# Kernel optimization log

Hardware: AMD Instinct MI355X
Metric: run time of the kernel (lower is better)

## Reference

```python
import jax, jax.numpy as jnp
import numpy as np

N = 100000   # nodes
R = 8        # relations
E = 150000   # edges per relation
D_IN = 128
D_OUT = 128
B = 2        # num_bases


def setup_inputs() -> dict:
    key = jax.random.key(0)
    ks = jax.random.split(key, 7)
    return {
        "x": jax.random.normal(ks[0], (N, D_IN), dtype=jnp.float32),
        "src": jax.random.randint(ks[1], (R, E), 0, N, dtype=jnp.int32),
        "dst": jax.random.randint(ks[2], (R, E), 0, N, dtype=jnp.int32),
        "basis_coeff": jax.random.normal(ks[3], (R, B), dtype=jnp.float32),
        "bases": jax.random.normal(ks[4], (B, D_IN, D_OUT), dtype=jnp.float32) * 0.05,
        "loop_weight": jax.random.normal(ks[5], (D_IN, D_OUT), dtype=jnp.float32) * 0.05,
        "h_bias": jax.random.normal(ks[6], (D_OUT,), dtype=jnp.float32) * 0.01,
    }


def reference(x, src, dst, basis_coeff, bases, loop_weight, h_bias):
    n = x.shape[0]
    # basis-decomposed per-relation weights: [R, D_IN, D_OUT]
    weight = jnp.einsum('rb,bio->rio', basis_coeff, bases)
    # gather src features per relation: [R, E, D_IN]
    msgs = x[src]
    # scatter-add onto dst nodes per relation (SpMM aggregate): [R, N, D_IN]
    agg = jax.vmap(lambda m, d: jax.ops.segment_sum(m, d, num_segments=n))(msgs, dst)
    # right normalization: divide by in-degree (clamped to 1), as in DGL GraphConv norm='right'
    ones = jnp.ones(src.shape[1], dtype=x.dtype)
    deg = jax.vmap(lambda d: jax.ops.segment_sum(ones, d, num_segments=n))(dst)
    agg = agg / jnp.clip(deg, 1.0)[..., None]
    # per-relation weight then sum across relations (HeteroGraphConv 'sum' agg)
    h = jnp.einsum('rni,rio->no', agg, weight)
    # self-loop + bias + activation (dropout = 0.0, eval)
    h = h + x @ loop_weight + h_bias
    return jax.nn.relu(h)
```

## Files before the change

kernel.cpp:

```cpp
#include <hip/hip_runtime.h>
#include <hip/hip_fp16.h>


#define DFEAT 128
#define NREL 8
#define ALDA 264

typedef __attribute__((ext_vector_type(8))) short bf16x8;
typedef __attribute__((ext_vector_type(4))) float f32x4;
typedef __attribute__((ext_vector_type(2))) float f32x2;

__device__ __forceinline__ ushort f2bf(float f) {
    unsigned u = __float_as_uint(f);
    u += 0x7FFF + ((u >> 16) & 1);
    return (ushort)(u >> 16);
}
__device__ __forceinline__ float bflo(unsigned u) { return __uint_as_float(u << 16); }
__device__ __forceinline__ float bfhi(unsigned u) { return __uint_as_float(u & 0xFFFF0000u); }
__device__ __forceinline__ unsigned pack2bf(float lo, float hi) {
    return (unsigned)f2bf(lo) | ((unsigned)f2bf(hi) << 16);
}

__global__ void fused_pre(const int* __restrict__ dst, int* __restrict__ deg,
                          ushort* __restrict__ rank,
                          const float* __restrict__ x, ushort* __restrict__ xb,
                          const float* __restrict__ bases, const float* __restrict__ loopw,
                          ushort* __restrict__ w2T,
                          int RE, int E, int N, int n4) {
    const int stride = gridDim.x * blockDim.x;
    const int t0 = blockIdx.x * blockDim.x + threadIdx.x;
    for (int i = t0; i < RE; i += stride) {
        int r = i / E;
        int d = dst[i];
        rank[i] = (ushort)atomicAdd(&deg[r * N + d], 1);
    }
    for (int i = t0; i < n4; i += stride) {
        float4 v = ((const float4*)x)[i];
        ushort4 o;
        o.x = f2bf(v.x); o.y = f2bf(v.y); o.z = f2bf(v.z); o.w = f2bf(v.w);
        ((ushort4*)xb)[i] = o;
    }
    for (int i = t0; i < 128 * 384; i += stride) {
        int j = i / 384, k = i % 384;
        float v = (k < 256) ? bases[(k >> 7) * DFEAT * DFEAT + (k & 127) * DFEAT + j]
                            : loopw[(k - 256) * DFEAT + j];
        w2T[i] = f2bf(v);
    }
}

__global__ void scan_block_sums(const int* __restrict__ deg, int* __restrict__ cnt,
                                int* __restrict__ bsums, int N) {
    __shared__ int sdata[256];
    int b = blockIdx.x, t = threadIdx.x;
    int idx = b * 256 + t;
    int sum = 0;
    if (idx < N) {
        #pragma unroll
        for (int r = 0; r < NREL; ++r) sum += deg[r * N + idx];
        cnt[idx] = sum;
    }
    sdata[t] = sum; __syncthreads();
    for (int s = 128; s > 0; s >>= 1) {
        if (t < s) sdata[t] += sdata[t + s];
        __syncthreads();
    }
    if (t == 0) bsums[b] = sdata[0];
}

__global__ void scan_mid(int* __restrict__ bsums, int nb) {
    __shared__ int s[256];
    int t = threadIdx.x;
    int base = t * 4;
    int v[4]; int sum = 0;
    #pragma unroll
    for (int i = 0; i < 4; ++i) {
        v[i] = sum;
        int c = (base + i < nb) ? bsums[base + i] : 0;
        sum += c;
    }
    s[t] = sum; __syncthreads();
    for (int off = 1; off < 256; off <<= 1) {
        int add = (t >= off) ? s[t - off] : 0;
        __syncthreads();
        s[t] += add;
        __syncthreads();
    }
    int excl = (t == 0) ? 0 : s[t - 1];
    #pragma unroll
    for (int i = 0; i < 4; ++i)
        if (base + i < nb) bsums[base + i] = excl + v[i];
}

__global__ void scan_write(const int* __restrict__ cnt, const int* __restrict__ bsums,
                           const int* __restrict__ deg,
                           int* __restrict__ rowStart, unsigned* __restrict__ packed,
                           int N) {
    __shared__ int tsum[256];
    int b = blockIdx.x, t = threadIdx.x;
    int idx = b * 256 + t;
    int c = (idx < N) ? cnt[idx] : 0;
    tsum[t] = c; __syncthreads();
    for (int off = 1; off < 256; off <<= 1) {
        int x = 0;
        if (t >= off) x = tsum[t - off];
        __syncthreads();
        if (t >= off) tsum[t] += x;
        __syncthreads();
    }
    int excl = (t == 0) ? 0 : tsum[t - 1];
    if (idx < N) {
        int rs = bsums[b] + excl;
        rowStart[idx] = rs;
        int pre = 0;
        #pragma unroll
        for (int r = 0; r < NREL; ++r) {
            int dv = deg[r * N + idx];
            packed[r * N + idx] = ((unsigned)(rs + pre) << 11) | (unsigned)dv;
            pre += dv;
        }
    }
}

__global__ void fill_kernel(const int* __restrict__ src, const int* __restrict__ dst,
                            const float* __restrict__ coeff,
                            const ushort* __restrict__ rank,
                            const unsigned* __restrict__ packed,
                            uint2* __restrict__ recs, int RE, int E, int N) {
    int idx = blockIdx.x * blockDim.x + threadIdx.x;
    if (idx >= RE) return;
    int r = idx / E;
    int d = dst[idx];
    unsigned p = packed[r * N + d];
    int pos = (int)(p >> 11) + (int)rank[idx];
    float inv = 1.0f / (float)(p & 2047u);
    __half2 hc = __floats2half2_rn(coeff[2 * r] * inv, coeff[2 * r + 1] * inv);
    uint2 rec;
    rec.x = (unsigned)src[idx];
    rec.y = *(unsigned*)&hc;
    recs[pos] = rec;
}

__global__ __launch_bounds__(256, 6) void gather_gemm(
    const uint2* __restrict__ recs, const int* __restrict__ rowStart,
    const int* __restrict__ cnt, const ushort* __restrict__ xb,
    const ushort* __restrict__ w2T, const float* __restrict__ bias,
    float* __restrict__ out, int N) {
    __shared__ __align__(16) ushort agg[32 * ALDA];
    const int tid = threadIdx.x;
    const int wave = tid >> 6, lane = tid & 63;
    const int q = lane >> 4;
    const int h = lane & 15;
    const int row0 = blockIdx.x * 32;

    for (int i = wave; i < 32; i += 4) {
        int d = row0 + i;
        if (d >= N) break;
        f32x2 A0 = {0.f, 0.f}, A1 = {0.f, 0.f}, A2 = {0.f, 0.f}, A3 = {0.f, 0.f};
        f32x2 B0 = {0.f, 0.f}, B1 = {0.f, 0.f}, B2 = {0.f, 0.f}, B3 = {0.f, 0.f};
        const int start = rowStart[d];
        const int len = cnt[d];
        for (int i2 = 0; i2 < len; i2 += 16) {
            uint2 r[4];
            #pragma unroll
            for (int j = 0; j < 4; ++j) {
                int e = i2 + 4 * j + q;
                r[j] = recs[start + (e < len ? e : len - 1)];
            }
            uint4 u[4];
            #pragma unroll
            for (int j = 0; j < 4; ++j)
                u[j] = *(const uint4*)(xb + (size_t)r[j].x * DFEAT + h * 8);
            #pragma unroll
            for (int j = 0; j < 4; ++j) {
                int e = i2 + 4 * j + q;
                __half2 hc = *(__half2*)&r[j].y;
                bool valid = e < len;
                float c0 = valid ? __low2float(hc) : 0.f;
                float c1 = valid ? __high2float(hc) : 0.f;
                f32x2 cc0 = {c0, c0}, cc1 = {c1, c1};
                uint4 uu = u[j];
                f32x2 f01 = {bflo(uu.x), bfhi(uu.x)};
                f32x2 f23 = {bflo(uu.y), bfhi(uu.y)};
                f32x2 f45 = {bflo(uu.z), bfhi(uu.z)};
                f32x2 f67 = {bflo(uu.w), bfhi(uu.w)};
                A0 += cc0 * f01; A1 += cc0 * f23; A2 += cc0 * f45; A3 += cc0 * f67;
                B0 += cc1 * f01; B1 += cc1 * f23; B2 += cc1 * f45; B3 += cc1 * f67;
            }
        }
        #define RED2(V) \
            V.x += __shfl_xor(V.x, 16); V.y += __shfl_xor(V.y, 16); \
            V.x += __shfl_xor(V.x, 32); V.y += __shfl_xor(V.y, 32);
        RED2(A0) RED2(A1) RED2(A2) RED2(A3)
        RED2(B0) RED2(B1) RED2(B2) RED2(B3)
        #undef RED2
        f32x2 W0 = q ? B0 : A0, W1 = q ? B1 : A1, W2 = q ? B2 : A2, W3 = q ? B3 : A3;
        uint4 w;
        w.x = pack2bf(W0.x, W0.y);
        w.y = pack2bf(W1.x, W1.y);
        w.z = pack2bf(W2.x, W2.y);
        w.w = pack2bf(W3.x, W3.y);
        if (q < 2)
            *(uint4*)(agg + i * ALDA + q * 128 + h * 8) = w;
    }
    __syncthreads();

    const int quad = lane >> 4, l16 = lane & 15;
    int arow[2];
    #pragma unroll
    for (int m = 0; m < 2; ++m) {
        int r = row0 + m * 16 + l16;
        arow[m] = (r < N) ? r : 0;
    }

    f32x4 zero = {0.f, 0.f, 0.f, 0.f};
    f32x4 acc[2][2] = {{zero, zero}, {zero, zero}};

    #pragma unroll
    for (int kt = 0; kt < 3; ++kt) {
        bf16x8 bq[4][2];
        #pragma unroll
        for (int t = 0; t < 4; ++t)
            #pragma unroll
            for (int g = 0; g < 2; ++g)
                bq[t][g] = *(const bf16x8*)(w2T + (size_t)(wave * 32 + g * 16 + l16) * 384
                                            + kt * 128 + t * 32 + quad * 8);
        #pragma unroll
        for (int m = 0; m < 2; ++m) {
            #pragma unroll
            for (int t = 0; t < 4; ++t) {
                bf16x8 a;
                if (kt < 2)
                    a = *(const bf16x8*)(agg + (m * 16 + l16) * ALDA + kt * 128 + t * 32 + quad * 8);
                else
                    a = *(const bf16x8*)(xb + (size_t)arow[m] * DFEAT + t * 32 + quad * 8);
                acc[m][0] = __builtin_amdgcn_mfma_f32_16x16x32_bf16(a, bq[t][0], acc[m][0], 0, 0, 0);
                acc[m][1] = __builtin_amdgcn_mfma_f32_16x16x32_bf16(a, bq[t][1], acc[m][1], 0, 0, 0);
            }
        }
    }

    #pragma unroll
    for (int g = 0; g < 2; ++g) {
        int c = wave * 32 + g * 16 + l16;
        float bv = bias[c];
        #pragma unroll
        for (int m = 0; m < 2; ++m) {
            #pragma unroll
            for (int reg = 0; reg < 4; ++reg) {
                int grow = row0 + m * 16 + quad * 4 + reg;
                if (grow < N)
                    out[(size_t)grow * DFEAT + c] = fmaxf(acc[m][g][reg] + bv, 0.f);
            }
        }
    }
}

extern "C" void kernel_launch(void* const* d_in, const int* in_sizes, int n_in,
                              void* d_out, int out_size, void* d_ws, size_t ws_size,
                              hipStream_t stream) {
    const float* x     = (const float*)d_in[0];
    const int*   src   = (const int*)  d_in[1];
    const int*   dst   = (const int*)  d_in[2];
    const float* coeff = (const float*)d_in[3];
    const float* bases = (const float*)d_in[4];
    const float* loopw = (const float*)d_in[5];
    const float* bias  = (const float*)d_in[6];
    float* out = (float*)d_out;

    const int N  = in_sizes[0] / DFEAT;
    const int RE = in_sizes[1];
    const int B  = in_sizes[4] / (DFEAT * DFEAT);
    const int R  = in_sizes[3] / B;
    const int E  = RE / R;
    const int NB = (N + 255) / 256;

    char* ws = (char*)d_ws;
    size_t off = 0;
    auto alloc = [&](size_t bytes) { void* p = ws + off; off = (off + bytes + 255) & ~(size_t)255; return p; };
    int*      deg      = (int*)     alloc((size_t)R * N * sizeof(int));
    ushort*   rank     = (ushort*)  alloc((size_t)RE * sizeof(ushort));
    unsigned* packed   = (unsigned*)alloc((size_t)R * N * sizeof(unsigned));
    int*      cnt      = (int*)     alloc((size_t)N * sizeof(int));
    int*      rowStart = (int*)     alloc((size_t)N * sizeof(int));
    int*      bsums    = (int*)     alloc((size_t)NB * sizeof(int));
    ushort*   w2T      = (ushort*)  alloc((size_t)128 * 384 * sizeof(ushort));
    ushort*   xb       = (ushort*)  alloc((size_t)N * DFEAT * sizeof(ushort));
    uint2*    recs     = (uint2*)   alloc((size_t)RE * sizeof(uint2));

    hipMemsetAsync(deg, 0, (size_t)R * N * sizeof(int), stream);
    fused_pre<<<4096, 256, 0, stream>>>(dst, deg, rank, x, xb, bases, loopw, w2T,
                                        RE, E, N, N * 32);
    scan_block_sums<<<NB, 256, 0, stream>>>(deg, cnt, bsums, N);
    scan_mid<<<1, 256, 0, stream>>>(bsums, NB);
    scan_write<<<NB, 256, 0, stream>>>(cnt, bsums, deg, rowStart, packed, N);
    fill_kernel<<<(RE + 255) / 256, 256, 0, stream>>>(src, dst, coeff, rank, packed,
                                                      recs, RE, E, N);

    gather_gemm<<<(N + 31) / 32, 256, 0, stream>>>(recs, rowStart, cnt, xb, w2T,
                                                   bias, out, N);
}
```

Before: 285.7 us.

## Balance edge gather across block with merge-path split and LDS float atomics

Rewrites the aggregation phase of gather_gemm so the block's contiguous edge range is split evenly among 16 thread groups, instead of assigning one destination row per wave. Each group walks its edges, tracking the local destination row encoded in the high bits of the record's src field, and flushes partial sums into an fp32 LDS tile with atomic adds. The aim is to remove load imbalance from variable in-degree and the padded, masked edge slots. In exchange it adds LDS zeroing, many LDS atomics, a serial dependent loop per thread with one edge per iteration, a larger fp32 shared tile with lower occupancy (launch bounds 6 to 4), and bf16 conversion at MFMA operand load.

Measured after the change: 408.6 us. +43.0%, slower.

```diff
diff --git a/kernel.cpp b/kernel.cpp
--- a/kernel.cpp
+++ b/kernel.cpp
@@ -4,7 +4,7 @@
 
 #define DFEAT 128
 #define NREL 8
-#define ALDA 264
+#define AF_LDA 260
 
 typedef __attribute__((ext_vector_type(8))) short bf16x8;
 typedef __attribute__((ext_vector_type(4))) float f32x4;
@@ -17,9 +17,6 @@
 }
 __device__ __forceinline__ float bflo(unsigned u) { return __uint_as_float(u << 16); }
 __device__ __forceinline__ float bfhi(unsigned u) { return __uint_as_float(u & 0xFFFF0000u); }
-__device__ __forceinline__ unsigned pack2bf(float lo, float hi) {
-    return (unsigned)f2bf(lo) | ((unsigned)f2bf(hi) << 16);
-}
 
 __global__ void fused_pre(const int* __restrict__ dst, int* __restrict__ deg,
                           ushort* __restrict__ rank,
@@ -135,72 +132,85 @@
     float inv = 1.0f / (float)(p & 2047u);
     __half2 hc = __floats2half2_rn(coeff[2 * r] * inv, coeff[2 * r + 1] * inv);
     uint2 rec;
-    rec.x = (unsigned)src[idx];
+    rec.x = (unsigned)src[idx] | ((unsigned)(d & 31) << 27);
     rec.y = *(unsigned*)&hc;
     recs[pos] = rec;
 }
 
-__global__ __launch_bounds__(256, 6) void gather_gemm(
+__global__ __launch_bounds__(256, 4) void gather_gemm(
     const uint2* __restrict__ recs, const int* __restrict__ rowStart,
-    const int* __restrict__ cnt, const ushort* __restrict__ xb,
+    const ushort* __restrict__ xb,
     const ushort* __restrict__ w2T, const float* __restrict__ bias,
-    float* __restrict__ out, int N) {
-    __shared__ __align__(16) ushort agg[32 * ALDA];
+    float* __restrict__ out, int N, int RE) {
+    __shared__ __align__(16) float aggf[32 * AF_LDA];
     const int tid = threadIdx.x;
     const int wave = tid >> 6, lane = tid & 63;
-    const int q = lane >> 4;
-    const int h = lane & 15;
     const int row0 = blockIdx.x * 32;
 
-    for (int i = wave; i < 32; i += 4) {
-        int d = row0 + i;
-        if (d >= N) break;
-        f32x2 A0 = {0.f, 0.f}, A1 = {0.f, 0.f}, A2 = {0.f, 0.f}, A3 = {0.f, 0.f};
-        f32x2 B0 = {0.f, 0.f}, B1 = {0.f, 0.f}, B2 = {0.f, 0.f}, B3 = {0.f, 0.f};
-        const int start = rowStart[d];
-        const int len = cnt[d];
-        for (int i2 = 0; i2 < len; i2 += 16) {
-            uint2 r[4];
-            #pragma unroll
-            for (int j = 0; j < 4; ++j) {
-                int e = i2 + 4 * j + q;
-                r[j] = recs[start + (e < len ? e : len - 1)];
-            }
-            uint4 u[4];
-            #pragma unroll
-            for (int j = 0; j < 4; ++j)
-                u[j] = *(const uint4*)(xb + (size_t)r[j].x * DFEAT + h * 8);
-            #pragma unroll
-            for (int j = 0; j < 4; ++j) {
-                int e = i2 + 4 * j + q;
-                __half2 hc = *(__half2*)&r[j].y;
-                bool valid = e < len;
-                float c0 = valid ? __low2float(hc) : 0.f;
-                float c1 = valid ? __high2float(hc) : 0.f;
+    {
+        uint4 z = {0u, 0u, 0u, 0u};
+        #pragma unroll
+        for (int i = 0; i < 9; ++i) {
+            int idx = tid + i * 256;
+            if (idx < (32 * AF_LDA) / 4)
+                ((uint4*)aggf)[idx] = z;
+        }
+    }
+    __syncthreads();
+
+    {
+        const int qb = tid >> 4;
+        const int h  = tid & 15;
+        const int e0 = rowStart[row0];
+        const int e1 = (row0 + 32 < N) ? rowStart[row0 + 32] : RE;
+        const int cntE = e1 - e0;
+        const int per = (cntE + 15) >> 4;
+        int qa = qb * per;      if (qa > cntE) qa = cntE;
+        int qe = qa + per;      if (qe > cntE) qe = cntE;
+        qa += e0; qe += e0;
+
+        f32x2 A0 = {0.f,0.f}, A1 = {0.f,0.f}, A2 = {0.f,0.f}, A3 = {0.f,0.f};
+        f32x2 B0 = {0.f,0.f}, B1 = {0.f,0.f}, B2 = {0.f,0.f}, B3 = {0.f,0.f};
+        int cur = -1;
+
+        #define FLUSH(C) { float* p = aggf + (C) * AF_LDA + h * 8;      \
+            atomicAdd(p + 0, A0.x);   atomicAdd(p + 1, A0.y);           \
+            atomicAdd(p + 2, A1.x);   atomicAdd(p + 3, A1.y);           \
+            atomicAdd(p + 4, A2.x);   atomicAdd(p + 5, A2.y);           \
+            atomicAdd(p + 6, A3.x);   atomicAdd(p + 7, A3.y);           \
+            atomicAdd(p + 128, B0.x); atomicAdd(p + 129, B0.y);         \
+            atomicAdd(p + 130, B1.x); atomicAdd(p + 131, B1.y);         \
+            atomicAdd(p + 132, B2.x); atomicAdd(p + 133, B2.y);         \
+            atomicAdd(p + 134, B3.x); atomicAdd(p + 135, B3.y); }
+
+        if (qa < qe) {
+            uint2 rec = recs[qa];
+            for (int e = qa; e < qe; ++e) {
+                uint2 nrec = rec;
+                if (e + 1 < qe) nrec = recs[e + 1];
+                unsigned srcI = rec.x & 0x07FFFFFFu;
+                int dloc = (int)(rec.x >> 27);
+                uint4 uu = *(const uint4*)(xb + (size_t)srcI * DFEAT + h * 8);
+                if (dloc != cur) {
+                    if (cur >= 0) FLUSH(cur)
+                    A0 = {0.f,0.f}; A1 = {0.f,0.f}; A2 = {0.f,0.f}; A3 = {0.f,0.f};
+                    B0 = {0.f,0.f}; B1 = {0.f,0.f}; B2 = {0.f,0.f}; B3 = {0.f,0.f};
+                    cur = dloc;
+                }
+                __half2 hc = *(__half2*)&rec.y;
+                float c0 = __low2float(hc), c1 = __high2float(hc);
                 f32x2 cc0 = {c0, c0}, cc1 = {c1, c1};
-                uint4 uu = u[j];
                 f32x2 f01 = {bflo(uu.x), bfhi(uu.x)};
                 f32x2 f23 = {bflo(uu.y), bfhi(uu.y)};
                 f32x2 f45 = {bflo(uu.z), bfhi(uu.z)};
                 f32x2 f67 = {bflo(uu.w), bfhi(uu.w)};
                 A0 += cc0 * f01; A1 += cc0 * f23; A2 += cc0 * f45; A3 += cc0 * f67;
                 B0 += cc1 * f01; B1 += cc1 * f23; B2 += cc1 * f45; B3 += cc1 * f67;
+                rec = nrec;
             }
-        }
-        #define RED2(V) \
-            V.x += __shfl_xor(V.x, 16); V.y += __shfl_xor(V.y, 16); \
-            V.x += __shfl_xor(V.x, 32); V.y += __shfl_xor(V.y, 32);
-        RED2(A0) RED2(A1) RED2(A2) RED2(A3)
-        RED2(B0) RED2(B1) RED2(B2) RED2(B3)
-        #undef RED2
-        f32x2 W0 = q ? B0 : A0, W1 = q ? B1 : A1, W2 = q ? B2 : A2, W3 = q ? B3 : A3;
-        uint4 w;
-        w.x = pack2bf(W0.x, W0.y);
-        w.y = pack2bf(W1.x, W1.y);
-        w.z = pack2bf(W2.x, W2.y);
-        w.w = pack2bf(W3.x, W3.y);
-        if (q < 2)
-            *(uint4*)(agg + i * ALDA + q * 128 + h * 8) = w;
+            FLUSH(cur)
+        }
+        #undef FLUSH
     }
     __syncthreads();
 
@@ -229,10 +239,20 @@
             #pragma unroll
             for (int t = 0; t < 4; ++t) {
                 bf16x8 a;
-                if (kt < 2)
-                    a = *(const bf16x8*)(agg + (m * 16 + l16) * ALDA + kt * 128 + t * 32 + quad * 8);
-                else
+                if (kt < 2) {
+                    const float* ap = aggf + (size_t)(m * 16 + l16) * AF_LDA
+                                      + kt * 128 + t * 32 + quad * 8;
+                    f32x4 lo = *(const f32x4*)ap;
+                    f32x4 hi = *(const f32x4*)(ap + 4);
+                    union { bf16x8 v; ushort s[8]; } ua;
+                    ua.s[0] = f2bf(lo.x); ua.s[1] = f2bf(lo.y);
+                    ua.s[2] = f2bf(lo.z); ua.s[3] = f2bf(lo.w);
+                    ua.s[4] = f2bf(hi.x); ua.s[5] = f2bf(hi.y);
+                    ua.s[6] = f2bf(hi.z); ua.s[7] = f2bf(hi.w);
+                    a = ua.v;
+                } else {
                     a = *(const bf16x8*)(xb + (size_t)arow[m] * DFEAT + t * 32 + quad * 8);
+                }
                 acc[m][0] = __builtin_amdgcn_mfma_f32_16x16x32_bf16(a, bq[t][0], acc[m][0], 0, 0, 0);
                 acc[m][1] = __builtin_amdgcn_mfma_f32_16x16x32_bf16(a, bq[t][1], acc[m][1], 0, 0, 0);
             }
@@ -296,6 +316,6 @@
     fill_kernel<<<(RE + 255) / 256, 256, 0, stream>>>(src, dst, coeff, rank, packed,
                                                       recs, RE, E, N);
 
-    gather_gemm<<<(N + 31) / 32, 256, 0, stream>>>(recs, rowStart, cnt, xb, w2T,
-                                                   bias, out, N);
-}
+    gather_gemm<<<(N + 31) / 32, 256, 0, stream>>>(recs, rowStart, xb, w2T,
+                                                   bias, out, N, RE);
+}
```

## Stage block edge records in LDS and assign one 16-lane group per node

Applied to the files above, without the earlier changes.

The gather phase now stages all edge records for the block's 32 destination rows into shared memory when they fit in a fixed capacity. It falls back to global reads otherwise. Each 16-lane group handles a whole node serially with 8 loads in flight, instead of a wave splitting a node's edges across 4 quarters. This removes the cross-quarter shuffle reductions and wasted lanes for low-degree nodes, but adds LDS usage, lowers the occupancy hint, and leaves more load imbalance across lanes of varying degree.

Result: no change. 285.8 us (+0.0%).

```diff
diff --git a/kernel.cpp b/kernel.cpp
--- a/kernel.cpp
+++ b/kernel.cpp
@@ -5,6 +5,7 @@
 #define DFEAT 128
 #define NREL 8
 #define ALDA 264
+#define ECAP 1024
 
 typedef __attribute__((ext_vector_type(8))) short bf16x8;
 typedef __attribute__((ext_vector_type(4))) float f32x4;
@@ -140,67 +141,90 @@
     recs[pos] = rec;
 }
 
-__global__ __launch_bounds__(256, 6) void gather_gemm(
+__global__ __launch_bounds__(256, 5) void gather_gemm(
     const uint2* __restrict__ recs, const int* __restrict__ rowStart,
-    const int* __restrict__ cnt, const ushort* __restrict__ xb,
+    const ushort* __restrict__ xb,
     const ushort* __restrict__ w2T, const float* __restrict__ bias,
-    float* __restrict__ out, int N) {
+    float* __restrict__ out, int N, int RE) {
     __shared__ __align__(16) ushort agg[32 * ALDA];
+    __shared__ __align__(16) uint2 recsL[ECAP];
+    __shared__ int rsl[33];
     const int tid = threadIdx.x;
     const int wave = tid >> 6, lane = tid & 63;
-    const int q = lane >> 4;
-    const int h = lane & 15;
     const int row0 = blockIdx.x * 32;
 
-    for (int i = wave; i < 32; i += 4) {
-        int d = row0 + i;
-        if (d >= N) break;
-        f32x2 A0 = {0.f, 0.f}, A1 = {0.f, 0.f}, A2 = {0.f, 0.f}, A3 = {0.f, 0.f};
-        f32x2 B0 = {0.f, 0.f}, B1 = {0.f, 0.f}, B2 = {0.f, 0.f}, B3 = {0.f, 0.f};
-        const int start = rowStart[d];
-        const int len = cnt[d];
-        for (int i2 = 0; i2 < len; i2 += 16) {
-            uint2 r[4];
-            #pragma unroll
-            for (int j = 0; j < 4; ++j) {
-                int e = i2 + 4 * j + q;
-                r[j] = recs[start + (e < len ? e : len - 1)];
+    if (tid < 33) {
+        int d = row0 + tid;
+        rsl[tid] = (d < N) ? rowStart[d] : RE;
+    }
+    __syncthreads();
+    const int e0 = rsl[0];
+    const int cntE = rsl[32] - e0;
+    const bool fits = (cntE <= ECAP);
+    {
+        const int lim = fits ? cntE : 0;
+        for (int k = tid; k < lim; k += 256)
+            recsL[k] = recs[e0 + k];
+    }
+    __syncthreads();
+
+    {
+        const int qw = tid >> 4;
+        const int h  = tid & 15;
+
+        auto gatherNode = [&](int i, auto getRec) {
+            const int s   = rsl[i] - e0;
+            const int len = rsl[i + 1] - rsl[i];
+            f32x2 A0 = {0.f,0.f}, A1 = {0.f,0.f}, A2 = {0.f,0.f}, A3 = {0.f,0.f};
+            f32x2 B0 = {0.f,0.f}, B1 = {0.f,0.f}, B2 = {0.f,0.f}, B3 = {0.f,0.f};
+            if (len > 0) {
+                const int last = s + len - 1;
+                for (int k = 0; k < len; k += 8) {
+                    uint2 rc[8];
+                    #pragma unroll
+                    for (int j = 0; j < 8; ++j) {
+                        int li = s + k + j;
+                        rc[j] = getRec(li <= last ? li : last);
+                    }
+                    uint4 u[8];
+                    #pragma unroll
+                    for (int j = 0; j < 8; ++j)
+                        u[j] = *(const uint4*)(xb + (size_t)rc[j].x * DFEAT + h * 8);
+                    #pragma unroll
+                    for (int j = 0; j < 8; ++j) {
+                        bool v = (k + j) < len;
+                        __half2 hc = *(__half2*)&rc[j].y;
+                        float c0 = v ? __low2float(hc) : 0.f;
+                        float c1 = v ? __high2float(hc) : 0.f;
+                        f32x2 cc0 = {c0, c0}, cc1 = {c1, c1};
+                        uint4 uu = u[j];
+                        f32x2 f01 = {bflo(uu.x), bfhi(uu.x)};
+                        f32x2 f23 = {bflo(uu.y), bfhi(uu.y)};
+                        f32x2 f45 = {bflo(uu.z), bfhi(uu.z)};
+                        f32x2 f67 = {bflo(uu.w), bfhi(uu.w)};
+                        A0 += cc0 * f01; A1 += cc0 * f23; A2 += cc0 * f45; A3 += cc0 * f67;
+                        B0 += cc1 * f01; B1 += cc1 * f23; B2 += cc1 * f45; B3 += cc1 * f67;
+                    }
+                }
             }
-            uint4 u[4];
-            #pragma unroll
-            for (int j = 0; j < 4; ++j)
-                u[j] = *(const uint4*)(xb + (size_t)r[j].x * DFEAT + h * 8);
-            #pragma unroll
-            for (int j = 0; j < 4; ++j) {
-                int e = i2 + 4 * j + q;
-                __half2 hc = *(__half2*)&r[j].y;
-                bool valid = e < len;
-                float c0 = valid ? __low2float(hc) : 0.f;
-                float c1 = valid ? __high2float(hc) : 0.f;
-                f32x2 cc0 = {c0, c0}, cc1 = {c1, c1};
-                uint4 uu = u[j];
-                f32x2 f01 = {bflo(uu.x), bfhi(uu.x)};
-                f32x2 f23 = {bflo(uu.y), bfhi(uu.y)};
-                f32x2 f45 = {bflo(uu.z), bfhi(uu.z)};
-                f32x2 f67 = {bflo(uu.w), bfhi(uu.w)};
-                A0 += cc0 * f01; A1 += cc0 * f23; A2 += cc0 * f45; A3 += cc0 * f67;
-                B0 += cc1 * f01; B1 += cc1 * f23; B2 += cc1 * f45; B3 += cc1 * f67;
-            }
+            uint4 w0, w1;
+            w0.x = pack2bf(A0.x, A0.y); w0.y = pack2bf(A1.x, A1.y);
+            w0.z = pack2bf(A2.x, A2.y); w0.w = pack2bf(A3.x, A3.y);
+            w1.x = pack2bf(B0.x, B0.y); w1.y = pack2bf(B1.x, B1.y);
+            w1.z = pack2bf(B2.x, B2.y); w1.w = pack2bf(B3.x, B3.y);
+            *(uint4*)(agg + i * ALDA + h * 8)       = w0;
+            *(uint4*)(agg + i * ALDA + 128 + h * 8) = w1;
+        };
+
+        if (fits) {
+            #pragma unroll
+            for (int p = 0; p < 2; ++p)
+                gatherNode(qw + p * 16, [&](int li) { return recsL[li]; });
+        } else {
+            #pragma unroll
+            for (int p = 0; p < 2; ++p)
+                gatherNode(qw + p * 16, [&](int li) { return recs[e0 + li]; });
         }
-        #define RED2(V) \
-            V.x += __shfl_xor(V.x, 16); V.y += __shfl_xor(V.y, 16); \
-            V.x += __shfl_xor(V.x, 32); V.y += __shfl_xor(V.y, 32);
-        RED2(A0) RED2(A1) RED2(A2) RED2(A3)
-        RED2(B0) RED2(B1) RED2(B2) RED2(B3)
-        #undef RED2
-        f32x2 W0 = q ? B0 : A0, W1 = q ? B1 : A1, W2 = q ? B2 : A2, W3 = q ? B3 : A3;
-        uint4 w;
-        w.x = pack2bf(W0.x, W0.y);
-        w.y = pack2bf(W1.x, W1.y);
-        w.z = pack2bf(W2.x, W2.y);
-        w.w = pack2bf(W3.x, W3.y);
-        if (q < 2)
-            *(uint4*)(agg + i * ALDA + q * 128 + h * 8) = w;
     }
     __syncthreads();
 
@@ -296,6 +320,6 @@
     fill_kernel<<<(RE + 255) / 256, 256, 0, stream>>>(src, dst, coeff, rank, packed,
                                                       recs, RE, E, N);
 
-    gather_gemm<<<(N + 31) / 32, 256, 0, stream>>>(recs, rowStart, cnt, xb, w2T,
-                                                   bias, out, N);
-}
+    gather_gemm<<<(N + 31) / 32, 256, 0, stream>>>(recs, rowStart, xb, w2T,
+                                                   bias, out, N, RE);
+}
```
